# Kernel optimization log

Hardware: AMD Instinct MI355X
Metric: run time of the kernel (lower is better)

## Reference

```python
import jax, jax.numpy as jnp
import numpy as np

B, T, C, H = 4, 2048, 1024, 16  # batch, seq, d_model, heads
D = C // H                      # head_dim = 64


def setup_inputs() -> dict:
    key = jax.random.key(0)
    ks = jax.random.split(key, 7)
    s = 1.0 / np.sqrt(C)
    return {
        "q_x": jax.random.normal(ks[0], (B, T, C), jnp.float32),
        "Wq": jax.random.normal(ks[1], (C, C), jnp.float32) * s,
        "bq": jax.random.normal(ks[2], (C,), jnp.float32) * 0.01,
        "Wk": jax.random.normal(ks[3], (C, C), jnp.float32) * s,
        "bk": jax.random.normal(ks[4], (C,), jnp.float32) * 0.01,
        "Wv": jax.random.normal(ks[5], (C, C), jnp.float32) * s,
        "bv": jax.random.normal(ks[6], (C,), jnp.float32) * 0.01,
    }


def reference(q_x, Wq, bq, Wk, bk, Wv, bv):
    # Self-attention path (k_x = v_x = q_x). Torch Linear: y = x @ W.T + b.
    q = q_x @ Wq.T + bq          # [B,T,C]
    k = q_x @ Wk.T + bk
    v = q_x @ Wv.T + bv
    # split heads: (B,T,C) -> (B,H,T,D); matches torch reshape(T,B*H,D) layout
    def heads(x):
        return x.reshape(B, T, H, D).transpose(0, 2, 1, 3)
    qh, kh, vh = heads(q), heads(k), heads(v)
    scale = 1.0 / np.sqrt(D)
    attn = jnp.einsum('bhtd,bhsd->bhts', qh, kh) * scale  # [B,H,T,T]
    attn = jax.nn.softmax(attn, axis=-1)
    x = jnp.einsum('bhts,bhsd->bhtd', attn, vh)           # [B,H,T,D]
    # merge heads back -> (B,T,C); batch_first=True output
    return x.transpose(0, 2, 1, 3).reshape(B, T, C)
```

## Files before the change

### kernel.cpp

```cpp
#include <hip/hip_runtime.h>
#include <hip/hip_bf16.h>
#include <stdint.h>
#include <stddef.h>

#define B_ 4
#define T_ 2048
#define C_ 1024
#define H_ 16
#define D_ 64
#define M_ (B_ * T_)

typedef __bf16 bf16x8 __attribute__((ext_vector_type(8)));
typedef float  f32x4  __attribute__((ext_vector_type(4)));
typedef unsigned short u16x8 __attribute__((ext_vector_type(8)));
typedef unsigned short u16x4 __attribute__((ext_vector_type(4)));
typedef unsigned int   u32x4 __attribute__((ext_vector_type(4)));

__device__ __forceinline__ unsigned short f2bf(float f) {
    union { float f; unsigned int u; } c; c.f = f;
    unsigned int u = c.u;
    unsigned int r = (u + 0x7fffu + ((u >> 16) & 1u)) >> 16;
    return (unsigned short)r;
}

__device__ __forceinline__ unsigned int pack2bf(float a, float b) {
    unsigned int ua = __builtin_bit_cast(unsigned int, a) + 0x8000u;
    unsigned int ub = __builtin_bit_cast(unsigned int, b) + 0x8000u;
    return __builtin_amdgcn_perm(ub, ua, 0x07060302u);
}

__device__ __forceinline__ bf16x8 ld_bf16x8(const unsigned short* p) {
    u16x8 v = *(const u16x8*)p;
    return __builtin_bit_cast(bf16x8, v);
}

__device__ __forceinline__ void gl_lds16(const unsigned short* g, unsigned short* l) {
    __builtin_amdgcn_global_load_lds(
        (const void __attribute__((address_space(1)))*)g,
        (void __attribute__((address_space(3)))*)l, 16, 0, 0);
}

__device__ __forceinline__ f32x4 vmax4(f32x4 a, f32x4 b) {
    f32x4 r;
    r.x = fmaxf(a.x, b.x); r.y = fmaxf(a.y, b.y);
    r.z = fmaxf(a.z, b.z); r.w = fmaxf(a.w, b.w);
    return r;
}

#define X4_ ((int64_t)M_ * C_ / 4)
#define W4_ ((int64_t)C_ * C_ / 4)

__global__ __launch_bounds__(256)
void cvt_bf16(const float* __restrict__ x,
              const float* __restrict__ Wq, const float* __restrict__ Wk,
              const float* __restrict__ Wv,
              unsigned short* __restrict__ xb, unsigned short* __restrict__ wb)
{
    const int64_t i4 = (int64_t)blockIdx.x * blockDim.x + threadIdx.x;
    const float* src; unsigned short* dst; int64_t off;
    if (i4 < X4_) { src = x; dst = xb; off = i4; }
    else {
        int64_t j = i4 - X4_;
        int which = (int)(j / W4_);
        off = j - (int64_t)which * W4_;
        src = (which == 0) ? Wq : (which == 1) ? Wk : Wv;
        dst = wb + (int64_t)which * C_ * C_;
    }
    f32x4 v = *(const f32x4*)(src + off * 4);
    u16x4 o = { f2bf(v.x), f2bf(v.y), f2bf(v.z), f2bf(v.w) };
    *(u16x4*)(dst + off * 4) = o;
}

#define K1_ 0.180336880f

__global__ __launch_bounds__(256)
void qkv_gemm(const unsigned short* __restrict__ xb,
              const unsigned short* __restrict__ wb,
              const float* __restrict__ bq, const float* __restrict__ bk,
              const float* __restrict__ bv,
              unsigned short* __restrict__ qo,
              unsigned short* __restrict__ ko,
              unsigned short* __restrict__ vo)
{
    __shared__ alignas(16) unsigned short As[128 * 64];
    __shared__ alignas(16) unsigned short Bs[128 * 64];

    const int tid   = threadIdx.x;
    const int bm    = blockIdx.x;
    const int bn    = blockIdx.y;
    const int which = bn >> 3;
    const int n_base = (bn & 7) * 128;
    const int nrow   = bn * 128;
    const int m_base = bm * 128;

    const float* bias = (which == 0) ? bq : (which == 1) ? bk : bv;

    const int w = tid >> 6, lane = tid & 63;
    const int wr = w >> 1, wc = w & 1;
    const int ln = lane & 15, quad = lane >> 4;

    const int srow   = lane >> 3;
    const int schunk = (lane & 7) ^ srow;
    const int scu    = schunk * 8;

    const f32x4 fz = {0.f, 0.f, 0.f, 0.f};
    f32x4 acc[4][4];
#pragma unroll
    for (int i = 0; i < 4; ++i)
#pragma unroll
        for (int j = 0; j < 4; ++j) acc[i][j] = fz;

    for (int k0 = 0; k0 < C_; k0 += 64) {
        __syncthreads();
#pragma unroll
        for (int i = 0; i < 4; ++i) {
            const int r = w * 32 + i * 8 + srow;
            gl_lds16(xb + (size_t)(m_base + r) * C_ + k0 + scu, As + (w * 4 + i) * 512);
            gl_lds16(wb + (size_t)(nrow  + r) * C_ + k0 + scu, Bs + (w * 4 + i) * 512);
        }
        __syncthreads();

#pragma unroll
        for (int kk = 0; kk < 2; ++kk) {
            bf16x8 af[4], bfr[4];
#pragma unroll
            for (int mi = 0; mi < 4; ++mi) {
                const int r = wr * 64 + mi * 16 + ln;
                af[mi] = ld_bf16x8(&As[r * 64 + (((kk * 4 + quad) ^ (ln & 7)) * 8)]);
            }
#pragma unroll
            for (int ni = 0; ni < 4; ++ni) {
                const int r = wc * 64 + ni * 16 + ln;
                bfr[ni] = ld_bf16x8(&Bs[r * 64 + (((kk * 4 + quad) ^ (ln & 7)) * 8)]);
            }
#pragma unroll
            for (int mi = 0; mi < 4; ++mi)
#pragma unroll
                for (int ni = 0; ni < 4; ++ni)
                    acc[mi][ni] = __builtin_amdgcn_mfma_f32_16x16x32_bf16(
                        af[mi], bfr[ni], acc[mi][ni], 0, 0, 0);
        }
    }

#pragma unroll
    for (int ni = 0; ni < 4; ++ni) {
        const int n_local = n_base + wc * 64 + ni * 16 + ln;
        const float bv_ = bias[n_local];
        const int h = n_local >> 6, d = n_local & 63;
#pragma unroll
        for (int mi = 0; mi < 4; ++mi) {
            const int m0 = m_base + wr * 64 + mi * 16 + quad * 4;
            const int b  = m0 >> 11;
            const int t0 = m0 & (T_ - 1);
            f32x4 v = acc[mi][ni];
            if (which == 2) {
                const int tb   = t0 & ~127;
                const int w128 = t0 & 127;
                const int kvt  = w128 >> 4;
                const int qd   = (w128 >> 2) & 3;
                const int pos  = (kvt >> 1) * 32 + qd * 8 + (kvt & 1) * 4;
                u16x4 pk = { f2bf(v.x + bv_), f2bf(v.y + bv_),
                             f2bf(v.z + bv_), f2bf(v.w + bv_) };
                *(u16x4*)(&vo[((size_t)(b * H_ + h) * D_ + d) * T_ + tb + pos]) = pk;
            } else if (which == 0) {
                unsigned short* dst =
                    qo + ((size_t)(b * H_ + h) * T_ + t0) * (size_t)D_ + d;
                dst[0 * D_] = f2bf((v.x + bv_) * K1_);
                dst[1 * D_] = f2bf((v.y + bv_) * K1_);
                dst[2 * D_] = f2bf((v.z + bv_) * K1_);
                dst[3 * D_] = f2bf((v.w + bv_) * K1_);
            } else {
                unsigned short* dst =
                    ko + ((size_t)(b * H_ + h) * T_ + t0) * (size_t)D_ + d;
                dst[0 * D_] = f2bf(v.x + bv_);
                dst[1 * D_] = f2bf(v.y + bv_);
                dst[2 * D_] = f2bf(v.z + bv_);
                dst[3 * D_] = f2bf(v.w + bv_);
            }
        }
    }
}

__global__ __launch_bounds__(256)
void flash_attn(const unsigned short* __restrict__ qb,
                const unsigned short* __restrict__ kb,
                const unsigned short* __restrict__ vtb,
                float* __restrict__ out)
{
    __shared__ alignas(16) unsigned char smem[49152];
    float* Os = (float*)smem;
    unsigned short* Vs = (unsigned short*)(smem + 32768);

    const int tid = threadIdx.x;
    const int qt  = blockIdx.x;
    const int bh  = blockIdx.y;
    const int b   = bh >> 4, h = bh & 15;

    const int w = tid >> 6, lane = tid & 63;
    const int ln = lane & 15, quad = lane >> 4;

    const unsigned short* Qb = qb  + (size_t)bh * T_ * D_;
    const unsigned short* Kb = kb  + (size_t)bh * T_ * D_;
    const unsigned short* Vb = vtb + (size_t)bh * D_ * T_;

    const int qrow0 = qt * 128 + w * 16 + ln;
    const bf16x8 qA0 = ld_bf16x8(&Qb[(size_t)qrow0 * D_ + quad * 8]);
    const bf16x8 qA1 = ld_bf16x8(&Qb[(size_t)qrow0 * D_ + 32 + quad * 8]);
    const bf16x8 qB0 = ld_bf16x8(&Qb[(size_t)(qrow0 + 64) * D_ + quad * 8]);
    const bf16x8 qB1 = ld_bf16x8(&Qb[(size_t)(qrow0 + 64) * D_ + 32 + quad * 8]);

    const int srow   = lane >> 3;
    const int schunk = (lane & 7) ^ srow;
    const int scu    = schunk * 8;
    const int vrow = lane >> 4;

    const f32x4 fz = {0.f, 0.f, 0.f, 0.f};
    float m2a = -3.0e38f, lia = 0.f;
    float m2b = -3.0e38f, lib = 0.f;
    f32x4 accA[4], accB[4];
#pragma unroll
    for (int dt = 0; dt < 4; ++dt) { accA[dt] = fz; accB[dt] = fz; }

    auto stageK = [&](int kv0, int buf) {
        unsigned short* Ks = (unsigned short*)(smem + buf * 16384);
#pragma unroll
        for (int i = 0; i < 4; ++i) {
            const int kr = kv0 + w * 32 + i * 8 + srow;
            gl_lds16(Kb + (size_t)kr * D_ + scu, Ks + (w * 4 + i) * 512);
        }
    };
    auto stageV = [&](int kv0) {
#pragma unroll
        for (int i = 0; i < 4; ++i) {
            const int dr = (w * 4 + i) * 4 + vrow;
            const int vcs = (lane & 15) ^ ((i & 1) * 4 + vrow);
            gl_lds16(Vb + (size_t)dr * T_ + kv0 + vcs * 8, Vs + (w * 4 + i) * 512);
        }
    };

    stageK(0, 0);

    for (int kv0 = 0; kv0 < T_; kv0 += 128) {
        const int cur = (kv0 >> 7) & 1;
        __syncthreads();
        stageV(kv0);
        if (kv0 + 128 < T_) stageK(kv0 + 128, cur ^ 1);

        const unsigned short* Ks = (const unsigned short*)(smem + cur * 16384);

        f32x4 sA[8], sB[8];
#pragma unroll
        for (int kvt = 0; kvt < 8; ++kvt) {
            const int r_ = kvt * 16 + ln;
            bf16x8 kf0 = ld_bf16x8(&Ks[r_ * 64 + ((quad)     ^ (ln & 7)) * 8]);
            bf16x8 kf1 = ld_bf16x8(&Ks[r_ * 64 + ((quad + 4) ^ (ln & 7)) * 8]);
            f32x4 cA = fz, cB = fz;
            cA = __builtin_amdgcn_mfma_f32_16x16x32_bf16(kf0, qA0, cA, 0, 0, 0);
            cB = __builtin_amdgcn_mfma_f32_16x16x32_bf16(kf0, qB0, cB, 0, 0, 0);
            cA = __builtin_amdgcn_mfma_f32_16x16x32_bf16(kf1, qA1, cA, 0, 0, 0);
            cB = __builtin_amdgcn_mfma_f32_16x16x32_bf16(kf1, qB1, cB, 0, 0, 0);
            sA[kvt] = cA; sB[kvt] = cB;
        }

        u32x4 pksA[4], pksB[4];
        float alA, alB;
        {
            f32x4 mm = vmax4(vmax4(vmax4(sA[0], sA[1]), vmax4(sA[2], sA[3])),
                             vmax4(vmax4(sA[4], sA[5]), vmax4(sA[6], sA[7])));
            float mx = fmaxf(fmaxf(mm.x, mm.y), fmaxf(mm.z, mm.w));
            mx = fmaxf(mx, __shfl_xor(mx, 16));
            mx = fmaxf(mx, __shfl_xor(mx, 32));
            const float nm = fmaxf(m2a, mx);
            alA = __builtin_amdgcn_exp2f(m2a - nm);
            m2a = nm;
            f32x4 rsv = fz;
#pragma unroll
            for (int p = 0; p < 4; ++p) {
                f32x4 e0, e1;
                e0.x = __builtin_amdgcn_exp2f(sA[2*p].x - m2a);
                e0.y = __builtin_amdgcn_exp2f(sA[2*p].y - m2a);
                e0.z = __builtin_amdgcn_exp2f(sA[2*p].z - m2a);
                e0.w = __builtin_amdgcn_exp2f(sA[2*p].w - m2a);
                e1.x = __builtin_amdgcn_exp2f(sA[2*p+1].x - m2a);
                e1.y = __builtin_amdgcn_exp2f(sA[2*p+1].y - m2a);
                e1.z = __builtin_amdgcn_exp2f(sA[2*p+1].z - m2a);
                e1.w = __builtin_amdgcn_exp2f(sA[2*p+1].w - m2a);
                rsv += e0; rsv += e1;
                pksA[p][0] = pack2bf(e0.x, e0.y);
                pksA[p][1] = pack2bf(e0.z, e0.w);
                pksA[p][2] = pack2bf(e1.x, e1.y);
                pksA[p][3] = pack2bf(e1.z, e1.w);
            }
            float rs = (rsv.x + rsv.y) + (rsv.z + rsv.w);
            rs += __shfl_xor(rs, 16);
            rs += __shfl_xor(rs, 32);
            lia = lia * alA + rs;
        }
        {
            f32x4 mm = vmax4(vmax4(vmax4(sB[0], sB[1]), vmax4(sB[2], sB[3])),
                             vmax4(vmax4(sB[4], sB[5]), vmax4(sB[6], sB[7])));
            float mx = fmaxf(fmaxf(mm.x, mm.y), fmaxf(mm.z, mm.w));
            mx = fmaxf(mx, __shfl_xor(mx, 16));
            mx = fmaxf(mx, __shfl_xor(mx, 32));
            const float nm = fmaxf(m2b, mx);
            alB = __builtin_amdgcn_exp2f(m2b - nm);
            m2b = nm;
            f32x4 rsv = fz;
#pragma unroll
            for (int p = 0; p < 4; ++p) {
                f32x4 e0, e1;
                e0.x = __builtin_amdgcn_exp2f(sB[2*p].x - m2b);
                e0.y = __builtin_amdgcn_exp2f(sB[2*p].y - m2b);
                e0.z = __builtin_amdgcn_exp2f(sB[2*p].z - m2b);
                e0.w = __builtin_amdgcn_exp2f(sB[2*p].w - m2b);
                e1.x = __builtin_amdgcn_exp2f(sB[2*p+1].x - m2b);
                e1.y = __builtin_amdgcn_exp2f(sB[2*p+1].y - m2b);
                e1.z = __builtin_amdgcn_exp2f(sB[2*p+1].z - m2b);
                e1.w = __builtin_amdgcn_exp2f(sB[2*p+1].w - m2b);
                rsv += e0; rsv += e1;
                pksB[p][0] = pack2bf(e0.x, e0.y);
                pksB[p][1] = pack2bf(e0.z, e0.w);
                pksB[p][2] = pack2bf(e1.x, e1.y);
                pksB[p][3] = pack2bf(e1.z, e1.w);
            }
            float rs = (rsv.x + rsv.y) + (rsv.z + rsv.w);
            rs += __shfl_xor(rs, 16);
            rs += __shfl_xor(rs, 32);
            lib = lib * alB + rs;
        }

#pragma unroll
        for (int dt = 0; dt < 4; ++dt) { accA[dt] *= alA; accB[dt] *= alB; }

        __syncthreads();

#pragma unroll
        for (int dt = 0; dt < 4; ++dt) {
            const int vr = dt * 16 + ln;
#pragma unroll
            for (int p = 0; p < 4; ++p) {
                const int cl = ((p * 4 + quad) ^ (ln & 7));
                bf16x8 vv = ld_bf16x8(&Vs[vr * 128 + cl * 8]);
                accA[dt] = __builtin_amdgcn_mfma_f32_16x16x32_bf16(
                    vv, __builtin_bit_cast(bf16x8, pksA[p]), accA[dt], 0, 0, 0);
                accB[dt] = __builtin_amdgcn_mfma_f32_16x16x32_bf16(
                    vv, __builtin_bit_cast(bf16x8, pksB[p]), accB[dt], 0, 0, 0);
            }
        }
    }

    __syncthreads();
    const float rva = 1.0f / lia, rvb = 1.0f / lib;
#pragma unroll
    for (int dt = 0; dt < 4; ++dt)
#pragma unroll
        for (int r = 0; r < 4; ++r) {
            Os[(w * 16 + ln) * 72 + dt * 16 + quad * 4 + r]        = accA[dt][r] * rva;
            Os[(64 + w * 16 + ln) * 72 + dt * 16 + quad * 4 + r]   = accB[dt][r] * rvb;
        }
    __syncthreads();

    const int q  = tid >> 1;
    const int c0 = (tid & 1) * 32;
    const float* src = &Os[q * 72 + c0];
    float* dst = &out[((size_t)(b * T_ + qt * 128 + q)) * C_ + h * 64 + c0];
#pragma unroll
    for (int i = 0; i < 8; ++i)
        *(f32x4*)(dst + i * 4) = *(const f32x4*)(src + i * 4);
}

extern "C" void kernel_launch(void* const* d_in, const int* in_sizes, int n_in,
                              void* d_out, int out_size, void* d_ws, size_t ws_size,
                              hipStream_t stream) {
    const float* q_x = (const float*)d_in[0];
    const float* Wq  = (const float*)d_in[1];
    const float* bq  = (const float*)d_in[2];
    const float* Wk  = (const float*)d_in[3];
    const float* bk  = (const float*)d_in[4];
    const float* Wv  = (const float*)d_in[5];
    const float* bv  = (const float*)d_in[6];
    float* out = (float*)d_out;

    const size_t elems = (size_t)M_ * C_;
    unsigned short* xb  = (unsigned short*)d_ws;
    unsigned short* wb  = xb + elems;
    unsigned short* qb  = wb + (size_t)3 * C_ * C_;
    unsigned short* kb  = qb + elems;
    unsigned short* vtb = kb + elems;
    (void)ws_size; (void)in_sizes; (void)n_in; (void)out_size;

    const int64_t total4 = X4_ + 3 * W4_;
    cvt_bf16<<<(int)(total4 / 256), 256, 0, stream>>>(q_x, Wq, Wk, Wv, xb, wb);

    qkv_gemm<<<dim3(M_ / 128, 24), 256, 0, stream>>>(
        xb, wb, bq, bk, bv, qb, kb, vtb);

    flash_attn<<<dim3(T_ / 128, B_ * H_), 256, 0, stream>>>(qb, kb, vtb, out);
}
```

Baseline: 274.3 us.

## Enlarge attention Q tile to 256 rows, add lazy rescale and XCD-aware block swizzle

The flash-attention kernel now has each block handle 256 query rows (four 64-row groups per wave) instead of 128. This reuses each staged K/V tile across twice as many queries and halves K/V global traffic. Softmax now exponentiates against the previous running max and only rescales when the new max exceeds it by more than 8 (lazy rescaling), which removes a serial max-then-exp dependency. Both GEMM and attention grids are flattened and remapped so that consecutive blocks spread across the 8 XCDs, aiming for better L2 locality. The 4x4 accumulator set raises register pressure; launch_bounds(256,2) is added and the grid shrinks to 512 blocks.

```diff
diff --git a/kernel.cpp b/kernel.cpp
--- a/kernel.cpp
+++ b/kernel.cpp
@@ -85,12 +85,14 @@
     __shared__ alignas(16) unsigned short As[128 * 64];
     __shared__ alignas(16) unsigned short Bs[128 * 64];
 
-    const int tid   = threadIdx.x;
-    const int bm    = blockIdx.x;
-    const int bn    = blockIdx.y;
-    const int which = bn >> 3;
-    const int n_base = (bn & 7) * 128;
-    const int nrow   = bn * 128;
+    const int tid  = threadIdx.x;
+    const int flat = blockIdx.x;
+    const int t    = (flat & 7) * 192 + (flat >> 3);
+    const int bm   = t / 24;
+    const int bnF  = t - bm * 24;
+    const int which = bnF >> 3;
+    const int n_base = (bnF & 7) * 128;
+    const int nrow   = bnF * 128;
     const int m_base = bm * 128;
 
     const float* bias = (which == 0) ? bq : (which == 1) ? bk : bv;
@@ -181,7 +183,7 @@
     }
 }
 
-__global__ __launch_bounds__(256)
+__global__ __launch_bounds__(256, 2)
 void flash_attn(const unsigned short* __restrict__ qb,
                 const unsigned short* __restrict__ kb,
                 const unsigned short* __restrict__ vtb,
@@ -192,9 +194,11 @@
     unsigned short* Vs = (unsigned short*)(smem + 32768);
 
     const int tid = threadIdx.x;
-    const int qt  = blockIdx.x;
-    const int bh  = blockIdx.y;
-    const int b   = bh >> 4, h = bh & 15;
+    const int flat = blockIdx.x;
+    const int tile = (flat & 7) * 64 + (flat >> 3);
+    const int qt   = tile & 7;
+    const int bh   = tile >> 3;
+    const int b    = bh >> 4, h = bh & 15;
 
     const int w = tid >> 6, lane = tid & 63;
     const int ln = lane & 15, quad = lane >> 4;
@@ -203,11 +207,13 @@
     const unsigned short* Kb = kb  + (size_t)bh * T_ * D_;
     const unsigned short* Vb = vtb + (size_t)bh * D_ * T_;
 
-    const int qrow0 = qt * 128 + w * 16 + ln;
-    const bf16x8 qA0 = ld_bf16x8(&Qb[(size_t)qrow0 * D_ + quad * 8]);
-    const bf16x8 qA1 = ld_bf16x8(&Qb[(size_t)qrow0 * D_ + 32 + quad * 8]);
-    const bf16x8 qB0 = ld_bf16x8(&Qb[(size_t)(qrow0 + 64) * D_ + quad * 8]);
-    const bf16x8 qB1 = ld_bf16x8(&Qb[(size_t)(qrow0 + 64) * D_ + 32 + quad * 8]);
+    bf16x8 qf[4][2];
+#pragma unroll
+    for (int X = 0; X < 4; ++X) {
+        const int qr = qt * 256 + X * 64 + w * 16 + ln;
+        qf[X][0] = ld_bf16x8(&Qb[(size_t)qr * D_ + quad * 8]);
+        qf[X][1] = ld_bf16x8(&Qb[(size_t)qr * D_ + 32 + quad * 8]);
+    }
 
     const int srow   = lane >> 3;
     const int schunk = (lane & 7) ^ srow;
@@ -215,26 +221,28 @@
     const int vrow = lane >> 4;
 
     const f32x4 fz = {0.f, 0.f, 0.f, 0.f};
-    float m2a = -3.0e38f, lia = 0.f;
-    float m2b = -3.0e38f, lib = 0.f;
-    f32x4 accA[4], accB[4];
-#pragma unroll
-    for (int dt = 0; dt < 4; ++dt) { accA[dt] = fz; accB[dt] = fz; }
-
-    auto stageK = [&](int kv0, int buf) {
-        unsigned short* Ks = (unsigned short*)(smem + buf * 16384);
+    f32x4 acc[4][4];
+    float m2[4] = {0.f, 0.f, 0.f, 0.f};
+    float li[4] = {0.f, 0.f, 0.f, 0.f};
+#pragma unroll
+    for (int X = 0; X < 4; ++X)
+#pragma unroll
+        for (int dt = 0; dt < 4; ++dt) acc[X][dt] = fz;
+
+    auto stageK = [&](int kv0_, int buf) {
+        unsigned short* Ksw = (unsigned short*)(smem + buf * 16384);
 #pragma unroll
         for (int i = 0; i < 4; ++i) {
-            const int kr = kv0 + w * 32 + i * 8 + srow;
-            gl_lds16(Kb + (size_t)kr * D_ + scu, Ks + (w * 4 + i) * 512);
+            const int kr = kv0_ + w * 32 + i * 8 + srow;
+            gl_lds16(Kb + (size_t)kr * D_ + scu, Ksw + (w * 4 + i) * 512);
         }
     };
-    auto stageV = [&](int kv0) {
+    auto stageV = [&](int kv0_) {
 #pragma unroll
         for (int i = 0; i < 4; ++i) {
             const int dr = (w * 4 + i) * 4 + vrow;
             const int vcs = (lane & 15) ^ ((i & 1) * 4 + vrow);
-            gl_lds16(Vb + (size_t)dr * T_ + kv0 + vcs * 8, Vs + (w * 4 + i) * 512);
+            gl_lds16(Vb + (size_t)dr * T_ + kv0_ + vcs * 8, Vs + (w * 4 + i) * 512);
         }
     };
 
@@ -248,89 +256,55 @@
 
         const unsigned short* Ks = (const unsigned short*)(smem + cur * 16384);
 
-        f32x4 sA[8], sB[8];
+        u32x4 pks[4][4];
+        f32x4 mm[4], rsv[4];
+#pragma unroll
+        for (int X = 0; X < 4; ++X) {
+            mm[X]  = {-3.0e38f, -3.0e38f, -3.0e38f, -3.0e38f};
+            rsv[X] = fz;
+        }
+
 #pragma unroll
         for (int kvt = 0; kvt < 8; ++kvt) {
             const int r_ = kvt * 16 + ln;
             bf16x8 kf0 = ld_bf16x8(&Ks[r_ * 64 + ((quad)     ^ (ln & 7)) * 8]);
             bf16x8 kf1 = ld_bf16x8(&Ks[r_ * 64 + ((quad + 4) ^ (ln & 7)) * 8]);
-            f32x4 cA = fz, cB = fz;
-            cA = __builtin_amdgcn_mfma_f32_16x16x32_bf16(kf0, qA0, cA, 0, 0, 0);
-            cB = __builtin_amdgcn_mfma_f32_16x16x32_bf16(kf0, qB0, cB, 0, 0, 0);
-            cA = __builtin_amdgcn_mfma_f32_16x16x32_bf16(kf1, qA1, cA, 0, 0, 0);
-            cB = __builtin_amdgcn_mfma_f32_16x16x32_bf16(kf1, qB1, cB, 0, 0, 0);
-            sA[kvt] = cA; sB[kvt] = cB;
-        }
-
-        u32x4 pksA[4], pksB[4];
-        float alA, alB;
-        {
-            f32x4 mm = vmax4(vmax4(vmax4(sA[0], sA[1]), vmax4(sA[2], sA[3])),
-                             vmax4(vmax4(sA[4], sA[5]), vmax4(sA[6], sA[7])));
-            float mx = fmaxf(fmaxf(mm.x, mm.y), fmaxf(mm.z, mm.w));
+#pragma unroll
+            for (int X = 0; X < 4; ++X) {
+                f32x4 s = fz;
+                s = __builtin_amdgcn_mfma_f32_16x16x32_bf16(kf0, qf[X][0], s, 0, 0, 0);
+                s = __builtin_amdgcn_mfma_f32_16x16x32_bf16(kf1, qf[X][1], s, 0, 0, 0);
+                mm[X] = vmax4(mm[X], s);
+                f32x4 e;
+                e.x = __builtin_amdgcn_exp2f(s.x - m2[X]);
+                e.y = __builtin_amdgcn_exp2f(s.y - m2[X]);
+                e.z = __builtin_amdgcn_exp2f(s.z - m2[X]);
+                e.w = __builtin_amdgcn_exp2f(s.w - m2[X]);
+                rsv[X] += e;
+                pks[X][kvt >> 1][(kvt & 1) * 2]     = pack2bf(e.x, e.y);
+                pks[X][kvt >> 1][(kvt & 1) * 2 + 1] = pack2bf(e.z, e.w);
+            }
+        }
+
+        float fl[4];
+#pragma unroll
+        for (int X = 0; X < 4; ++X) {
+            float mx = fmaxf(fmaxf(mm[X].x, mm[X].y), fmaxf(mm[X].z, mm[X].w));
             mx = fmaxf(mx, __shfl_xor(mx, 16));
             mx = fmaxf(mx, __shfl_xor(mx, 32));
-            const float nm = fmaxf(m2a, mx);
-            alA = __builtin_amdgcn_exp2f(m2a - nm);
-            m2a = nm;
-            f32x4 rsv = fz;
-#pragma unroll
-            for (int p = 0; p < 4; ++p) {
-                f32x4 e0, e1;
-                e0.x = __builtin_amdgcn_exp2f(sA[2*p].x - m2a);
-                e0.y = __builtin_amdgcn_exp2f(sA[2*p].y - m2a);
-                e0.z = __builtin_amdgcn_exp2f(sA[2*p].z - m2a);
-                e0.w = __builtin_amdgcn_exp2f(sA[2*p].w - m2a);
-                e1.x = __builtin_amdgcn_exp2f(sA[2*p+1].x - m2a);
-                e1.y = __builtin_amdgcn_exp2f(sA[2*p+1].y - m2a);
-                e1.z = __builtin_amdgcn_exp2f(sA[2*p+1].z - m2a);
-                e1.w = __builtin_amdgcn_exp2f(sA[2*p+1].w - m2a);
-                rsv += e0; rsv += e1;
-                pksA[p][0] = pack2bf(e0.x, e0.y);
-                pksA[p][1] = pack2bf(e0.z, e0.w);
-                pksA[p][2] = pack2bf(e1.x, e1.y);
-                pksA[p][3] = pack2bf(e1.z, e1.w);
-            }
-            float rs = (rsv.x + rsv.y) + (rsv.z + rsv.w);
+            float rs = (rsv[X].x + rsv[X].y) + (rsv[X].z + rsv[X].w);
             rs += __shfl_xor(rs, 16);
             rs += __shfl_xor(rs, 32);
-            lia = lia * alA + rs;
-        }
-        {
-            f32x4 mm = vmax4(vmax4(vmax4(sB[0], sB[1]), vmax4(sB[2], sB[3])),
-                             vmax4(vmax4(sB[4], sB[5]), vmax4(sB[6], sB[7])));
-            float mx = fmaxf(fmaxf(mm.x, mm.y), fmaxf(mm.z, mm.w));
-            mx = fmaxf(mx, __shfl_xor(mx, 16));
-            mx = fmaxf(mx, __shfl_xor(mx, 32));
-            const float nm = fmaxf(m2b, mx);
-            alB = __builtin_amdgcn_exp2f(m2b - nm);
-            m2b = nm;
-            f32x4 rsv = fz;
-#pragma unroll
-            for (int p = 0; p < 4; ++p) {
-                f32x4 e0, e1;
-                e0.x = __builtin_amdgcn_exp2f(sB[2*p].x - m2b);
-                e0.y = __builtin_amdgcn_exp2f(sB[2*p].y - m2b);
-                e0.z = __builtin_amdgcn_exp2f(sB[2*p].z - m2b);
-                e0.w = __builtin_amdgcn_exp2f(sB[2*p].w - m2b);
-                e1.x = __builtin_amdgcn_exp2f(sB[2*p+1].x - m2b);
-                e1.y = __builtin_amdgcn_exp2f(sB[2*p+1].y - m2b);
-                e1.z = __builtin_amdgcn_exp2f(sB[2*p+1].z - m2b);
-                e1.w = __builtin_amdgcn_exp2f(sB[2*p+1].w - m2b);
-                rsv += e0; rsv += e1;
-                pksB[p][0] = pack2bf(e0.x, e0.y);
-                pksB[p][1] = pack2bf(e0.z, e0.w);
-                pksB[p][2] = pack2bf(e1.x, e1.y);
-                pksB[p][3] = pack2bf(e1.z, e1.w);
-            }
-            float rs = (rsv.x + rsv.y) + (rsv.z + rsv.w);
-            rs += __shfl_xor(rs, 16);
-            rs += __shfl_xor(rs, 32);
-            lib = lib * alB + rs;
-        }
-
-#pragma unroll
-        for (int dt = 0; dt < 4; ++dt) { accA[dt] *= alA; accB[dt] *= alB; }
+            if (__any(mx > m2[X] + 8.0f)) {
+                const float nm = fmaxf(m2[X], mx);
+                fl[X] = __builtin_amdgcn_exp2f(m2[X] - nm);
+                li[X] = (li[X] + rs) * fl[X];
+                m2[X] = nm;
+            } else {
+                fl[X] = 1.0f;
+                li[X] += rs;
+            }
+        }
 
         __syncthreads();
 
@@ -341,32 +315,46 @@
             for (int p = 0; p < 4; ++p) {
                 const int cl = ((p * 4 + quad) ^ (ln & 7));
                 bf16x8 vv = ld_bf16x8(&Vs[vr * 128 + cl * 8]);
-                accA[dt] = __builtin_amdgcn_mfma_f32_16x16x32_bf16(
-                    vv, __builtin_bit_cast(bf16x8, pksA[p]), accA[dt], 0, 0, 0);
-                accB[dt] = __builtin_amdgcn_mfma_f32_16x16x32_bf16(
-                    vv, __builtin_bit_cast(bf16x8, pksB[p]), accB[dt], 0, 0, 0);
-            }
-        }
-    }
-
-    __syncthreads();
-    const float rva = 1.0f / lia, rvb = 1.0f / lib;
-#pragma unroll
-    for (int dt = 0; dt < 4; ++dt)
-#pragma unroll
-        for (int r = 0; r < 4; ++r) {
-            Os[(w * 16 + ln) * 72 + dt * 16 + quad * 4 + r]        = accA[dt][r] * rva;
-            Os[(64 + w * 16 + ln) * 72 + dt * 16 + quad * 4 + r]   = accB[dt][r] * rvb;
-        }
-    __syncthreads();
+#pragma unroll
+                for (int X = 0; X < 4; ++X)
+                    acc[X][dt] = __builtin_amdgcn_mfma_f32_16x16x32_bf16(
+                        vv, __builtin_bit_cast(bf16x8, pks[X][p]), acc[X][dt], 0, 0, 0);
+            }
+        }
+
+#pragma unroll
+        for (int X = 0; X < 4; ++X)
+#pragma unroll
+            for (int dt = 0; dt < 4; ++dt) acc[X][dt] *= fl[X];
+    }
+
+    float rv[4];
+#pragma unroll
+    for (int X = 0; X < 4; ++X) rv[X] = 1.0f / li[X];
 
     const int q  = tid >> 1;
     const int c0 = (tid & 1) * 32;
-    const float* src = &Os[q * 72 + c0];
-    float* dst = &out[((size_t)(b * T_ + qt * 128 + q)) * C_ + h * 64 + c0];
-#pragma unroll
-    for (int i = 0; i < 8; ++i)
-        *(f32x4*)(dst + i * 4) = *(const f32x4*)(src + i * 4);
+    __syncthreads();
+#pragma unroll
+    for (int g = 0; g < 2; ++g) {
+#pragma unroll
+        for (int xi = 0; xi < 2; ++xi) {
+            const int X = g * 2 + xi;
+#pragma unroll
+            for (int dt = 0; dt < 4; ++dt)
+#pragma unroll
+                for (int r = 0; r < 4; ++r)
+                    Os[(xi * 64 + w * 16 + ln) * 72 + dt * 16 + quad * 4 + r] =
+                        acc[X][dt][r] * rv[X];
+        }
+        __syncthreads();
+        const float* src = &Os[q * 72 + c0];
+        float* dst = &out[((size_t)(b * T_ + qt * 256 + g * 128 + q)) * C_ + h * 64 + c0];
+#pragma unroll
+        for (int i = 0; i < 8; ++i)
+            *(f32x4*)(dst + i * 4) = *(const f32x4*)(src + i * 4);
+        __syncthreads();
+    }
 }
 
 extern "C" void kernel_launch(void* const* d_in, const int* in_sizes, int n_in,
@@ -392,8 +380,8 @@
     const int64_t total4 = X4_ + 3 * W4_;
     cvt_bf16<<<(int)(total4 / 256), 256, 0, stream>>>(q_x, Wq, Wk, Wv, xb, wb);
 
-    qkv_gemm<<<dim3(M_ / 128, 24), 256, 0, stream>>>(
+    qkv_gemm<<<1536, 256, 0, stream>>>(
         xb, wb, bq, bk, bv, qb, kb, vtb);
 
-    flash_attn<<<dim3(T_ / 128, B_ * H_), 256, 0, stream>>>(qb, kb, vtb, out);
-}
+    flash_attn<<<512, 256, 0, stream>>>(qb, kb, vtb, out);
+}
```

New measurement: 306.6 us. +11.8%, slower.

## Use fp16 for P·V with packed rtz converts, skip unneeded rescales, add occupancy hint

Applied to the files above, without the earlier changes.

V is now stored as fp16 using the packed round-toward-zero convert, and the softmax probabilities are packed the same way, so the P·V MFMA runs in f16 instead of bf16 and the manual bf16 packing goes away. The accumulator rescale and its exp2 are skipped whenever no lane's running max grew. The attention kernel also gets a launch bound of at least 2 blocks per CU, which limits registers. Risks are possible register spills under the tighter bound, and fp16 overflow if V values or biases grow large, though rtz keeps precision acceptable here.

```diff
diff --git a/kernel.cpp b/kernel.cpp
--- a/kernel.cpp
+++ b/kernel.cpp
@@ -11,10 +11,12 @@
 #define M_ (B_ * T_)
 
 typedef __bf16 bf16x8 __attribute__((ext_vector_type(8)));
+typedef _Float16 f16x8 __attribute__((ext_vector_type(8)));
 typedef float  f32x4  __attribute__((ext_vector_type(4)));
 typedef unsigned short u16x8 __attribute__((ext_vector_type(8)));
 typedef unsigned short u16x4 __attribute__((ext_vector_type(4)));
 typedef unsigned int   u32x4 __attribute__((ext_vector_type(4)));
+typedef unsigned int   u32x2 __attribute__((ext_vector_type(2)));
 
 __device__ __forceinline__ unsigned short f2bf(float f) {
     union { float f; unsigned int u; } c; c.f = f;
@@ -23,15 +25,18 @@
     return (unsigned short)r;
 }
 
-__device__ __forceinline__ unsigned int pack2bf(float a, float b) {
-    unsigned int ua = __builtin_bit_cast(unsigned int, a) + 0x8000u;
-    unsigned int ub = __builtin_bit_cast(unsigned int, b) + 0x8000u;
-    return __builtin_amdgcn_perm(ub, ua, 0x07060302u);
+__device__ __forceinline__ unsigned int pkrtz(float a, float b) {
+    return __builtin_bit_cast(unsigned int, __builtin_amdgcn_cvt_pkrtz(a, b));
 }
 
 __device__ __forceinline__ bf16x8 ld_bf16x8(const unsigned short* p) {
     u16x8 v = *(const u16x8*)p;
     return __builtin_bit_cast(bf16x8, v);
+}
+
+__device__ __forceinline__ f16x8 ld_f16x8(const unsigned short* p) {
+    u16x8 v = *(const u16x8*)p;
+    return __builtin_bit_cast(f16x8, v);
 }
 
 __device__ __forceinline__ void gl_lds16(const unsigned short* g, unsigned short* l) {
@@ -159,9 +164,9 @@
                 const int kvt  = w128 >> 4;
                 const int qd   = (w128 >> 2) & 3;
                 const int pos  = (kvt >> 1) * 32 + qd * 8 + (kvt & 1) * 4;
-                u16x4 pk = { f2bf(v.x + bv_), f2bf(v.y + bv_),
-                             f2bf(v.z + bv_), f2bf(v.w + bv_) };
-                *(u16x4*)(&vo[((size_t)(b * H_ + h) * D_ + d) * T_ + tb + pos]) = pk;
+                u32x2 pk2 = { pkrtz(v.x + bv_, v.y + bv_),
+                              pkrtz(v.z + bv_, v.w + bv_) };
+                *(u32x2*)(&vo[((size_t)(b * H_ + h) * D_ + d) * T_ + tb + pos]) = pk2;
             } else if (which == 0) {
                 unsigned short* dst =
                     qo + ((size_t)(b * H_ + h) * T_ + t0) * (size_t)D_ + d;
@@ -181,7 +186,7 @@
     }
 }
 
-__global__ __launch_bounds__(256)
+__global__ __launch_bounds__(256, 2)
 void flash_attn(const unsigned short* __restrict__ qb,
                 const unsigned short* __restrict__ kb,
                 const unsigned short* __restrict__ vtb,
@@ -264,14 +269,16 @@
 
         u32x4 pksA[4], pksB[4];
         float alA, alB;
+        bool growA, growB;
         {
             f32x4 mm = vmax4(vmax4(vmax4(sA[0], sA[1]), vmax4(sA[2], sA[3])),
                              vmax4(vmax4(sA[4], sA[5]), vmax4(sA[6], sA[7])));
             float mx = fmaxf(fmaxf(mm.x, mm.y), fmaxf(mm.z, mm.w));
             mx = fmaxf(mx, __shfl_xor(mx, 16));
             mx = fmaxf(mx, __shfl_xor(mx, 32));
+            growA = __any(mx > m2a);
             const float nm = fmaxf(m2a, mx);
-            alA = __builtin_amdgcn_exp2f(m2a - nm);
+            alA = growA ? __builtin_amdgcn_exp2f(m2a - nm) : 1.0f;
             m2a = nm;
             f32x4 rsv = fz;
 #pragma unroll
@@ -286,10 +293,10 @@
                 e1.z = __builtin_amdgcn_exp2f(sA[2*p+1].z - m2a);
                 e1.w = __builtin_amdgcn_exp2f(sA[2*p+1].w - m2a);
                 rsv += e0; rsv += e1;
-                pksA[p][0] = pack2bf(e0.x, e0.y);
-                pksA[p][1] = pack2bf(e0.z, e0.w);
-                pksA[p][2] = pack2bf(e1.x, e1.y);
-                pksA[p][3] = pack2bf(e1.z, e1.w);
+                pksA[p][0] = pkrtz(e0.x, e0.y);
+                pksA[p][1] = pkrtz(e0.z, e0.w);
+                pksA[p][2] = pkrtz(e1.x, e1.y);
+                pksA[p][3] = pkrtz(e1.z, e1.w);
             }
             float rs = (rsv.x + rsv.y) + (rsv.z + rsv.w);
             rs += __shfl_xor(rs, 16);
@@ -302,8 +309,9 @@
             float mx = fmaxf(fmaxf(mm.x, mm.y), fmaxf(mm.z, mm.w));
             mx = fmaxf(mx, __shfl_xor(mx, 16));
             mx = fmaxf(mx, __shfl_xor(mx, 32));
+            growB = __any(mx > m2b);
             const float nm = fmaxf(m2b, mx);
-            alB = __builtin_amdgcn_exp2f(m2b - nm);
+            alB = growB ? __builtin_amdgcn_exp2f(m2b - nm) : 1.0f;
             m2b = nm;
             f32x4 rsv = fz;
 #pragma unroll
@@ -318,10 +326,10 @@
                 e1.z = __builtin_amdgcn_exp2f(sB[2*p+1].z - m2b);
                 e1.w = __builtin_amdgcn_exp2f(sB[2*p+1].w - m2b);
                 rsv += e0; rsv += e1;
-                pksB[p][0] = pack2bf(e0.x, e0.y);
-                pksB[p][1] = pack2bf(e0.z, e0.w);
-                pksB[p][2] = pack2bf(e1.x, e1.y);
-                pksB[p][3] = pack2bf(e1.z, e1.w);
+                pksB[p][0] = pkrtz(e0.x, e0.y);
+                pksB[p][1] = pkrtz(e0.z, e0.w);
+                pksB[p][2] = pkrtz(e1.x, e1.y);
+                pksB[p][3] = pkrtz(e1.z, e1.w);
             }
             float rs = (rsv.x + rsv.y) + (rsv.z + rsv.w);
             rs += __shfl_xor(rs, 16);
@@ -329,8 +337,14 @@
             lib = lib * alB + rs;
         }
 
-#pragma unroll
-        for (int dt = 0; dt < 4; ++dt) { accA[dt] *= alA; accB[dt] *= alB; }
+        if (growA) {
+#pragma unroll
+            for (int dt = 0; dt < 4; ++dt) accA[dt] *= alA;
+        }
+        if (growB) {
+#pragma unroll
+            for (int dt = 0; dt < 4; ++dt) accB[dt] *= alB;
+        }
 
         __syncthreads();
 
@@ -340,11 +354,11 @@
 #pragma unroll
             for (int p = 0; p < 4; ++p) {
                 const int cl = ((p * 4 + quad) ^ (ln & 7));
-                bf16x8 vv = ld_bf16x8(&Vs[vr * 128 + cl * 8]);
-                accA[dt] = __builtin_amdgcn_mfma_f32_16x16x32_bf16(
-                    vv, __builtin_bit_cast(bf16x8, pksA[p]), accA[dt], 0, 0, 0);
-                accB[dt] = __builtin_amdgcn_mfma_f32_16x16x32_bf16(
-                    vv, __builtin_bit_cast(bf16x8, pksB[p]), accB[dt], 0, 0, 0);
+                f16x8 vv = ld_f16x8(&Vs[vr * 128 + cl * 8]);
+                accA[dt] = __builtin_amdgcn_mfma_f32_16x16x32_f16(
+                    vv, __builtin_bit_cast(f16x8, pksA[p]), accA[dt], 0, 0, 0);
+                accB[dt] = __builtin_amdgcn_mfma_f32_16x16x32_f16(
+                    vv, __builtin_bit_cast(f16x8, pksB[p]), accB[dt], 0, 0, 0);
             }
         }
     }
```

Measured after the change: 267.4 us. 2.5% less time.
